# Performance work log

Measured on AMD Instinct MI355X. Metric: run time of the kernel, lower is better.

## Reference

```python
import jax, jax.numpy as jnp
import numpy as np

N_NODES = 50000
N_EDGES = 1000000
D_FEAT = 512
F_ATTN = 64
SLOPE = 0.2


def setup_inputs() -> dict:
    key = jax.random.key(0)
    ks = jax.random.split(key, 8)
    d_sim = jax.random.normal(ks[0], (N_NODES, D_FEAT), dtype=jnp.float32)
    m_sim = jax.random.normal(ks[1], (N_NODES, D_FEAT), dtype=jnp.float32)
    Wd = jax.random.normal(ks[2], (F_ATTN, D_FEAT), dtype=jnp.float32) * (1.0 / np.sqrt(D_FEAT))
    Wm = jax.random.normal(ks[3], (F_ATTN, D_FEAT), dtype=jnp.float32) * (1.0 / np.sqrt(D_FEAT))
    Wa = jax.random.normal(ks[4], (2 * F_ATTN,), dtype=jnp.float32) * (1.0 / np.sqrt(2 * F_ATTN))
    node_type = jax.random.randint(ks[5], (N_NODES,), 0, 2, dtype=jnp.int32)
    edge_src = jax.random.randint(ks[6], (N_EDGES,), 0, N_NODES, dtype=jnp.int32)
    edge_dst = jax.random.randint(ks[7], (N_EDGES,), 0, N_NODES, dtype=jnp.int32)
    return {"d_sim": d_sim, "m_sim": m_sim, "Wd": Wd, "Wm": Wm, "Wa": Wa,
            "node_type": node_type, "edge_src": edge_src, "edge_dst": edge_dst}


def reference(d_sim, m_sim, Wd, Wm, Wa, node_type, edge_src, edge_dst):
    # Per-node projection, type-dependent (type==1 -> disease fc, type==0 -> miRNA fc).
    # Dropout is 0.0 (identity).
    z_d = d_sim @ Wd.T                      # [N, F]
    z_m = m_sim @ Wm.T                      # [N, F]
    z = jnp.where(node_type[:, None] == 1, z_d, z_m)  # [N, F]

    # Edge attention: a = attn_fc(concat(z_src, z_dst)); split Wa to avoid materializing concat.
    zs = z[edge_src]                        # [E, F]
    e = zs @ Wa[:F_ATTN] + z[edge_dst] @ Wa[F_ATTN:]  # [E]
    e = jax.nn.leaky_relu(e, negative_slope=SLOPE)

    # Segment softmax over incoming edges of each dst node (DGL mailbox softmax).
    emax = jax.ops.segment_max(e, edge_dst, num_segments=N_NODES)  # [N]
    ex = jnp.exp(e - emax[edge_dst])                                # [E]
    denom = jax.ops.segment_sum(ex, edge_dst, num_segments=N_NODES)  # [N]
    alpha = ex / denom[edge_dst]                                    # [E]

    # Weighted neighbor aggregation + elu.
    h = jax.ops.segment_sum(alpha[:, None] * zs, edge_dst, num_segments=N_NODES)  # [N, F]
    return jax.nn.elu(h)
```

## Files before the change

### kernel.cpp

```cpp
#include <hip/hip_runtime.h>
#include <hip/hip_bf16.h>

#define N_NODES 50000
#define N_EDGES 1000000
#define D_FEAT 512
#define F_ATTN 64
#define SLOPE 0.2f
#define CAP 64
#define BINS 391
#define BINCAP 4096
#define BINBLK 123
#define EPB 8192

typedef __attribute__((ext_vector_type(8))) short short8;
typedef __attribute__((ext_vector_type(4))) float floatx4;

static __device__ __forceinline__ short f2bf(float x) {
    unsigned u = __float_as_uint(x);
    unsigned r = (u + 0x7FFFu + ((u >> 16) & 1u)) >> 16;
    return (short)r;
}

static __device__ __forceinline__ short8 cvt2(float4 x, float4 y) {
    short8 r;
    r[0] = f2bf(x.x); r[1] = f2bf(x.y); r[2] = f2bf(x.z); r[3] = f2bf(x.w);
    r[4] = f2bf(y.x); r[5] = f2bf(y.y); r[6] = f2bf(y.z); r[7] = f2bf(y.w);
    return r;
}

static __device__ __forceinline__ float bfu2f(unsigned short v) {
    return __uint_as_float((unsigned)v << 16);
}

static __device__ __forceinline__ void g2lds16(const void* g, void* l) {
    __builtin_amdgcn_global_load_lds(
        (const __attribute__((address_space(1))) void*)g,
        (__attribute__((address_space(3))) void*)l, 16, 0, 0);
}

__global__ __launch_bounds__(256) void wcvt_kernel(
    const float* __restrict__ Wd, const float* __restrict__ Wm,
    short* __restrict__ Wb, int* __restrict__ gcount)
{
    int i = blockIdx.x * 256 + threadIdx.x;
    int half = F_ATTN * D_FEAT;
    float v = (i < half) ? Wd[i] : Wm[i - half];
    Wb[i] = f2bf(v);
    if (i < BINS) gcount[i] = 0;
}

__global__ __launch_bounds__(1024) void bin_kernel(
    const int* __restrict__ edge_src, const int* __restrict__ edge_dst,
    int* __restrict__ gcount, int* __restrict__ bins)
{
    __shared__ int hist[BINS];
    __shared__ int base[BINS];
    int tid = threadIdx.x;
    if (tid < BINS) hist[tid] = 0;
    __syncthreads();

    int e0 = blockIdx.x * EPB + tid * 8;
    int myV[8], myB[8], myR[8];
    if (e0 + 8 <= N_EDGES) {
        int4 d0 = *(const int4*)(edge_dst + e0);
        int4 d1 = *(const int4*)(edge_dst + e0 + 4);
        int4 s0 = *(const int4*)(edge_src + e0);
        int4 s1v = *(const int4*)(edge_src + e0 + 4);
        int dd[8] = {d0.x, d0.y, d0.z, d0.w, d1.x, d1.y, d1.z, d1.w};
        int ss[8] = {s0.x, s0.y, s0.z, s0.w, s1v.x, s1v.y, s1v.z, s1v.w};
        #pragma unroll
        for (int k = 0; k < 8; k++) {
            myV[k] = (ss[k] << 7) | (dd[k] & 127);
            myB[k] = dd[k] >> 7;
            myR[k] = atomicAdd(&hist[myB[k]], 1);
        }
    } else {
        #pragma unroll
        for (int k = 0; k < 8; k++) {
            int e = e0 + k;
            if (e < N_EDGES) {
                int d = edge_dst[e];
                int s = edge_src[e];
                myV[k] = (s << 7) | (d & 127);
                myB[k] = d >> 7;
                myR[k] = atomicAdd(&hist[myB[k]], 1);
            } else { myV[k] = -1; myB[k] = 0; myR[k] = 0; }
        }
    }
    __syncthreads();
    if (tid < BINS) {
        int c = hist[tid];
        base[tid] = c ? atomicAdd(&gcount[tid], c) : 0;
    }
    __syncthreads();
    #pragma unroll
    for (int k = 0; k < 8; k++) {
        if (myV[k] >= 0) {
            int pos = base[myB[k]] + myR[k];
            if (pos < BINCAP) bins[(myB[k] << 12) + pos] = myV[k];
        }
    }
}

__global__ __launch_bounds__(256) void proj_kernel(
    const float* __restrict__ d_sim,
    const float* __restrict__ m_sim,
    const short* __restrict__ Wb,
    const float* __restrict__ Wa,
    const int* __restrict__ node_type,
    __hip_bfloat16* __restrict__ z,
    float* __restrict__ s1, float* __restrict__ s2)
{
    __shared__ char smem[65536];

    const int w      = threadIdx.x >> 6;
    const int lane   = threadIdx.x & 63;
    const int laneLo = lane & 15;
    const int quad   = lane >> 4;
    const int nodeBase = blockIdx.x * 64;

    const float* aP[4];
    #pragma unroll
    for (int i = 0; i < 4; i++) {
        int r = w * 16 + i * 4 + (lane >> 4);
        int arow = nodeBase + r; if (arow >= N_NODES) arow = N_NODES - 1;
        int lc = (lane & 15) ^ (r & 7);
        const float* src = (node_type[arow] == 1) ? d_sim : m_sim;
        aP[i] = src + (size_t)arow * D_FEAT + (lc << 2);
    }
    const short* bP[4];
    #pragma unroll
    for (int i = 0; i < 4; i++) {
        int r = (w * 4 + i) * 8 + (lane >> 3);
        int lc = (lane & 7) ^ (r & 7);
        bP[i] = Wb + (size_t)r * D_FEAT + (lc << 3);
    }

    floatx4 accD[4], accM[4];
    #pragma unroll
    for (int nt = 0; nt < 4; nt++) {
        accD[nt] = (floatx4){0.f, 0.f, 0.f, 0.f};
        accM[nt] = (floatx4){0.f, 0.f, 0.f, 0.f};
    }

    {
        char* b0 = smem;
        #pragma unroll
        for (int i = 0; i < 4; i++)
            g2lds16(aP[i], b0 + (w * 16 + i * 4) * 256);
        #pragma unroll
        for (int i = 0; i < 4; i++)
            g2lds16(bP[i], b0 + 16384 + (w * 4 + i) * 1024);
    }
    __syncthreads();

    const int rA  = w * 16 + laneLo;
    const int rx  = laneLo & 7;

    for (int t = 0; t < 8; t++) {
        if (t < 7) {
            char* nb = smem + ((t + 1) & 1) * 32768;
            int k0 = (t + 1) * 64;
            #pragma unroll
            for (int i = 0; i < 4; i++)
                g2lds16(aP[i] + k0, nb + (w * 16 + i * 4) * 256);
            #pragma unroll
            for (int i = 0; i < 4; i++)
                g2lds16(bP[i] + k0, nb + 16384 + (w * 4 + i) * 1024);
        }
        const char* cb = smem + (t & 1) * 32768;
        #pragma unroll
        for (int ks = 0; ks < 2; ks++) {
            int c0 = ks * 8 + quad * 2;
            float4 a0 = *(const float4*)(cb + rA * 256 + ((c0 ^ rx) << 4));
            float4 a1 = *(const float4*)(cb + rA * 256 + (((c0 + 1) ^ rx) << 4));
            short8 a = cvt2(a0, a1);
            int ch = ks * 4 + quad;
            int sl = (ch ^ rx) << 4;
            #pragma unroll
            for (int nt = 0; nt < 4; nt++) {
                const char* rowD = cb + 16384 + (nt * 16 + laneLo) * 128;
                short8 bD = *(const short8*)(rowD + sl);
                short8 bM = *(const short8*)(rowD + 64 * 128 + sl);
                accD[nt] = __builtin_amdgcn_mfma_f32_16x16x32_bf16(a, bD, accD[nt], 0, 0, 0);
                accM[nt] = __builtin_amdgcn_mfma_f32_16x16x32_bf16(a, bM, accM[nt], 0, 0, 0);
            }
        }
        __syncthreads();
    }

    float wa1[4], wa2[4];
    #pragma unroll
    for (int nt = 0; nt < 4; nt++) {
        wa1[nt] = Wa[nt * 16 + laneLo];
        wa2[nt] = Wa[F_ATTN + nt * 16 + laneLo];
    }

    #pragma unroll
    for (int reg = 0; reg < 4; reg++) {
        int node = nodeBase + w * 16 + quad * 4 + reg;
        bool ok = node < N_NODES;
        int isD = ok ? (node_type[node] == 1) : 0;
        float p1 = 0.f, p2 = 0.f;
        #pragma unroll
        for (int nt = 0; nt < 4; nt++) {
            float v = isD ? accD[nt][reg] : accM[nt][reg];
            if (ok) z[(size_t)node * F_ATTN + nt * 16 + laneLo] = __float2bfloat16(v);
            p1 += v * wa1[nt];
            p2 += v * wa2[nt];
        }
        #pragma unroll
        for (int off = 8; off; off >>= 1) {
            p1 += __shfl_xor(p1, off);
            p2 += __shfl_xor(p2, off);
        }
        if (ok && laneLo == 0) { s1[node] = p1; s2[node] = p2; }
    }
}

__global__ __launch_bounds__(1024) void agg_kernel(
    const int* __restrict__ gcount, const int* __restrict__ bins,
    const float* __restrict__ s1, const float* __restrict__ s2,
    const __hip_bfloat16* __restrict__ z, float* __restrict__ out)
{
    __shared__ unsigned short list[128 * CAP];
    __shared__ int lcnt[128];
    __shared__ float sW[16 * 64];
    __shared__ int   sS[16 * 64];
    int tid = threadIdx.x;
    int b   = blockIdx.x;
    if (tid < 128) lcnt[tid] = 0;
    __syncthreads();

    int bc = gcount[b]; if (bc > BINCAP) bc = BINCAP;
    for (int i = tid; i < bc; i += 1024) {
        int v = bins[(b << 12) + i];
        int n = v & 127;
        int s = v >> 7;
        int r = atomicAdd(&lcnt[n], 1);
        if (r < CAP) list[(n << 6) + r] = (unsigned short)s;
    }
    __syncthreads();

    int wv    = tid >> 6;
    int lane  = tid & 63;
    int fgrp  = (lane & 15) * 4;
    int ep    = lane >> 4;
    int wbase = wv * 64;

    for (int j8 = 0; j8 < 8; j8++) {
        int ln   = wv * 8 + j8;
        int node = (b << 7) + ln;
        bool nvalid = node < N_NODES;
        int cnt = nvalid ? lcnt[ln] : 0;
        if (cnt > CAP) cnt = CAP;

        int   src = 0;
        float wgt = 0.f;
        if (lane < cnt) {
            src = list[(ln << 6) + lane];
            float t = s1[src] + s2[node];
            float ev = (t > 0.f) ? t : SLOPE * t;
            wgt = __expf(ev);
        }
        float l = wgt;
        sW[wbase + lane] = wgt;
        sS[wbase + lane] = src;

        float4 h = {0.f, 0.f, 0.f, 0.f};
        for (int j = 0; j < cnt; j += 16) {
            #pragma unroll
            for (int u = 0; u < 16; u += 4) {
                int slot = wbase + j + u + ep;
                float wj = sW[slot];
                int   sj = sS[slot];
                ushort4 zz = *(const ushort4*)((const unsigned short*)z +
                                               (size_t)sj * F_ATTN + fgrp);
                h.x += wj * bfu2f(zz.x);
                h.y += wj * bfu2f(zz.y);
                h.z += wj * bfu2f(zz.z);
                h.w += wj * bfu2f(zz.w);
            }
        }
        #pragma unroll
        for (int off = 16; off <= 32; off <<= 1) {
            h.x += __shfl_xor(h.x, off);
            h.y += __shfl_xor(h.y, off);
            h.z += __shfl_xor(h.z, off);
            h.w += __shfl_xor(h.w, off);
        }
        #pragma unroll
        for (int off = 32; off; off >>= 1) l += __shfl_xor(l, off);

        if (ep == 0 && nvalid) {
            float inv = (cnt > 0) ? 1.f / l : 0.f;
            float4 o;
            float v;
            v = h.x * inv; o.x = (v > 0.f) ? v : (__expf(v) - 1.f);
            v = h.y * inv; o.y = (v > 0.f) ? v : (__expf(v) - 1.f);
            v = h.z * inv; o.z = (v > 0.f) ? v : (__expf(v) - 1.f);
            v = h.w * inv; o.w = (v > 0.f) ? v : (__expf(v) - 1.f);
            *(float4*)(out + (size_t)node * F_ATTN + fgrp) = o;
        }
    }
}

extern "C" void kernel_launch(void* const* d_in, const int* in_sizes, int n_in,
                              void* d_out, int out_size, void* d_ws, size_t ws_size,
                              hipStream_t stream) {
    const float* d_sim = (const float*)d_in[0];
    const float* m_sim = (const float*)d_in[1];
    const float* Wd    = (const float*)d_in[2];
    const float* Wm    = (const float*)d_in[3];
    const float* Wa    = (const float*)d_in[4];
    const int* node_type = (const int*)d_in[5];
    const int* edge_src  = (const int*)d_in[6];
    const int* edge_dst  = (const int*)d_in[7];
    float* out = (float*)d_out;

    char* ws = (char*)d_ws;
    __hip_bfloat16* z  = (__hip_bfloat16*)(ws + 0);
    float* s1          = (float*)(ws + 6400000);
    float* s2          = (float*)(ws + 6600000);
    int*   gcount      = (int*)  (ws + 6800000);
    short* Wb          = (short*)(ws + 7000000);
    int*   bins        = (int*)  (ws + 8388608);

    wcvt_kernel<<<(2 * F_ATTN * D_FEAT) / 256, 256, 0, stream>>>(Wd, Wm, Wb, gcount);
    bin_kernel<<<BINBLK, 1024, 0, stream>>>(edge_src, edge_dst, gcount, bins);
    proj_kernel<<<(N_NODES + 63) / 64, 256, 0, stream>>>(
        d_sim, m_sim, Wb, Wa, node_type, z, s1, s2);
    agg_kernel<<<BINS, 1024, 0, stream>>>(gcount, bins, s1, s2, z, out);
}
```

Baseline: 259.8 us.

## Fuse edge binning into projection kernel via interleaved block roles

Merges the edge-binning kernel and the node projection GEMM into one launch. Blocks are assigned a role by an interleaved pattern (5 bin blocks per 13), so memory-bound binning overlaps with the compute-bound projection and one launch is saved. Bin blocks now use 256 threads over 2048 edges each. The aggregation inner loop is also changed to step by 4 slots instead of 16, which skips padded slots when a node has few neighbours. The cost is that bin blocks reserve the projection's 64KB of shared memory, which may reduce occupancy for them.

```diff
diff --git a/kernel.cpp b/kernel.cpp
--- a/kernel.cpp
+++ b/kernel.cpp
@@ -9,8 +9,10 @@
 #define CAP 64
 #define BINS 391
 #define BINCAP 4096
-#define BINBLK 123
-#define EPB 8192
+#define NPROJ 782
+#define NBINBLK 489
+#define EPB2 2048
+#define NB_TOT (NPROJ + NBINBLK)
 
 typedef __attribute__((ext_vector_type(8))) short short8;
 typedef __attribute__((ext_vector_type(4))) float floatx4;
@@ -49,75 +51,83 @@
     if (i < BINS) gcount[i] = 0;
 }
 
-__global__ __launch_bounds__(1024) void bin_kernel(
-    const int* __restrict__ edge_src, const int* __restrict__ edge_dst,
-    int* __restrict__ gcount, int* __restrict__ bins)
-{
-    __shared__ int hist[BINS];
-    __shared__ int base[BINS];
-    int tid = threadIdx.x;
-    if (tid < BINS) hist[tid] = 0;
-    __syncthreads();
-
-    int e0 = blockIdx.x * EPB + tid * 8;
-    int myV[8], myB[8], myR[8];
-    if (e0 + 8 <= N_EDGES) {
-        int4 d0 = *(const int4*)(edge_dst + e0);
-        int4 d1 = *(const int4*)(edge_dst + e0 + 4);
-        int4 s0 = *(const int4*)(edge_src + e0);
-        int4 s1v = *(const int4*)(edge_src + e0 + 4);
-        int dd[8] = {d0.x, d0.y, d0.z, d0.w, d1.x, d1.y, d1.z, d1.w};
-        int ss[8] = {s0.x, s0.y, s0.z, s0.w, s1v.x, s1v.y, s1v.z, s1v.w};
-        #pragma unroll
-        for (int k = 0; k < 8; k++) {
-            myV[k] = (ss[k] << 7) | (dd[k] & 127);
-            myB[k] = dd[k] >> 7;
-            myR[k] = atomicAdd(&hist[myB[k]], 1);
-        }
-    } else {
-        #pragma unroll
-        for (int k = 0; k < 8; k++) {
-            int e = e0 + k;
-            if (e < N_EDGES) {
-                int d = edge_dst[e];
-                int s = edge_src[e];
-                myV[k] = (s << 7) | (d & 127);
-                myB[k] = d >> 7;
-                myR[k] = atomicAdd(&hist[myB[k]], 1);
-            } else { myV[k] = -1; myB[k] = 0; myR[k] = 0; }
-        }
-    }
-    __syncthreads();
-    if (tid < BINS) {
-        int c = hist[tid];
-        base[tid] = c ? atomicAdd(&gcount[tid], c) : 0;
-    }
-    __syncthreads();
-    #pragma unroll
-    for (int k = 0; k < 8; k++) {
-        if (myV[k] >= 0) {
-            int pos = base[myB[k]] + myR[k];
-            if (pos < BINCAP) bins[(myB[k] << 12) + pos] = myV[k];
-        }
-    }
-}
-
-__global__ __launch_bounds__(256) void proj_kernel(
+__global__ __launch_bounds__(256) void fused_kernel(
     const float* __restrict__ d_sim,
     const float* __restrict__ m_sim,
     const short* __restrict__ Wb,
     const float* __restrict__ Wa,
     const int* __restrict__ node_type,
+    const int* __restrict__ edge_src,
+    const int* __restrict__ edge_dst,
     __hip_bfloat16* __restrict__ z,
-    float* __restrict__ s1, float* __restrict__ s2)
+    float* __restrict__ s1, float* __restrict__ s2,
+    int* __restrict__ gcount, int* __restrict__ bins)
 {
     __shared__ char smem[65536];
 
-    const int w      = threadIdx.x >> 6;
-    const int lane   = threadIdx.x & 63;
+    const int bid = blockIdx.x;
+    const int tid = threadIdx.x;
+    const int r13 = bid % 13;
+    const int nbBefore = (bid / 13) * 5 + (r13 < 5 ? r13 : 5);
+    const bool isBin = (r13 < 5) && (nbBefore < NBINBLK);
+
+    if (isBin) {
+        int* hist = (int*)smem;
+        int* base = (int*)(smem + 4096);
+        const int q = nbBefore;
+        for (int i = tid; i < BINS; i += 256) hist[i] = 0;
+        __syncthreads();
+
+        int e0 = q * EPB2 + tid * 8;
+        int myV[8], myB[8], myR[8];
+        if (e0 + 8 <= N_EDGES) {
+            int4 d0 = *(const int4*)(edge_dst + e0);
+            int4 d1 = *(const int4*)(edge_dst + e0 + 4);
+            int4 s0 = *(const int4*)(edge_src + e0);
+            int4 s1v = *(const int4*)(edge_src + e0 + 4);
+            int dd[8] = {d0.x, d0.y, d0.z, d0.w, d1.x, d1.y, d1.z, d1.w};
+            int ss[8] = {s0.x, s0.y, s0.z, s0.w, s1v.x, s1v.y, s1v.z, s1v.w};
+            #pragma unroll
+            for (int k = 0; k < 8; k++) {
+                myV[k] = (ss[k] << 7) | (dd[k] & 127);
+                myB[k] = dd[k] >> 7;
+                myR[k] = atomicAdd(&hist[myB[k]], 1);
+            }
+        } else {
+            #pragma unroll
+            for (int k = 0; k < 8; k++) {
+                int e = e0 + k;
+                if (e < N_EDGES) {
+                    int d = edge_dst[e];
+                    int s = edge_src[e];
+                    myV[k] = (s << 7) | (d & 127);
+                    myB[k] = d >> 7;
+                    myR[k] = atomicAdd(&hist[myB[k]], 1);
+                } else { myV[k] = -1; myB[k] = 0; myR[k] = 0; }
+            }
+        }
+        __syncthreads();
+        for (int i = tid; i < BINS; i += 256) {
+            int c = hist[i];
+            base[i] = c ? atomicAdd(&gcount[i], c) : 0;
+        }
+        __syncthreads();
+        #pragma unroll
+        for (int k = 0; k < 8; k++) {
+            if (myV[k] >= 0) {
+                int pos = base[myB[k]] + myR[k];
+                if (pos < BINCAP) bins[(myB[k] << 12) + pos] = myV[k];
+            }
+        }
+        return;
+    }
+
+    const int p      = bid - (nbBefore < NBINBLK ? nbBefore : NBINBLK);
+    const int w      = tid >> 6;
+    const int lane   = tid & 63;
     const int laneLo = lane & 15;
     const int quad   = lane >> 4;
-    const int nodeBase = blockIdx.x * 64;
+    const int nodeBase = p * 64;
 
     const float* aP[4];
     #pragma unroll
@@ -268,19 +278,17 @@
         sS[wbase + lane] = src;
 
         float4 h = {0.f, 0.f, 0.f, 0.f};
-        for (int j = 0; j < cnt; j += 16) {
-            #pragma unroll
-            for (int u = 0; u < 16; u += 4) {
-                int slot = wbase + j + u + ep;
-                float wj = sW[slot];
-                int   sj = sS[slot];
-                ushort4 zz = *(const ushort4*)((const unsigned short*)z +
-                                               (size_t)sj * F_ATTN + fgrp);
-                h.x += wj * bfu2f(zz.x);
-                h.y += wj * bfu2f(zz.y);
-                h.z += wj * bfu2f(zz.z);
-                h.w += wj * bfu2f(zz.w);
-            }
+        int usteps = (cnt + 3) >> 2;
+        for (int uu = 0; uu < usteps; uu++) {
+            int slot = wbase + (uu << 2) + ep;
+            float wj = sW[slot];
+            int   sj = sS[slot];
+            ushort4 zz = *(const ushort4*)((const unsigned short*)z +
+                                           (size_t)sj * F_ATTN + fgrp);
+            h.x += wj * bfu2f(zz.x);
+            h.y += wj * bfu2f(zz.y);
+            h.z += wj * bfu2f(zz.z);
+            h.w += wj * bfu2f(zz.w);
         }
         #pragma unroll
         for (int off = 16; off <= 32; off <<= 1) {
@@ -327,8 +335,8 @@
     int*   bins        = (int*)  (ws + 8388608);
 
     wcvt_kernel<<<(2 * F_ATTN * D_FEAT) / 256, 256, 0, stream>>>(Wd, Wm, Wb, gcount);
-    bin_kernel<<<BINBLK, 1024, 0, stream>>>(edge_src, edge_dst, gcount, bins);
-    proj_kernel<<<(N_NODES + 63) / 64, 256, 0, stream>>>(
-        d_sim, m_sim, Wb, Wa, node_type, z, s1, s2);
+    fused_kernel<<<NB_TOT, 256, 0, stream>>>(
+        d_sim, m_sim, Wb, Wa, node_type, edge_src, edge_dst,
+        z, s1, s2, gcount, bins);
     agg_kernel<<<BINS, 1024, 0, stream>>>(gcount, bins, s1, s2, z, out);
 }
```

After: 253.9 us. 1.02x faster.
